# Optimization experiments

Hardware: AMD Instinct MI355X
Metric: run time of the kernel (lower is better)

Reference implementation:

```python
import jax, jax.numpy as jnp
import numpy as np

PAD = 0
C_CONST = 0.1712209


def setup_inputs() -> dict:
    key = jax.random.key(0)
    ks = jax.random.split(key, 6)
    tlen, bsz, slen, hsize, vocab = 64, 32, 64, 1024, 32000
    hidden = jax.random.normal(ks[0], (tlen, bsz, hsize), dtype=jnp.float32)
    context = jax.random.normal(ks[1], (slen, bsz, hsize), dtype=jnp.float32)
    src = jax.random.randint(ks[2], (bsz, slen), 0, vocab, dtype=jnp.int64)
    stdv = 1.0 / np.sqrt(hsize)
    W_gen = jax.random.uniform(ks[3], (vocab, hsize), dtype=jnp.float32, minval=-stdv, maxval=stdv)
    b_gen = jnp.zeros((vocab,), dtype=jnp.float32)
    # Xavier-like init for the copy gate
    w_copy = jax.random.normal(ks[4], (hsize,), dtype=jnp.float32) * np.sqrt(2.0 / (hsize + 1))
    b_copy = jnp.zeros((1,), dtype=jnp.float32)
    return {"hidden": hidden, "context": context, "src": src,
            "W_gen": W_gen, "b_gen": b_gen, "w_copy": w_copy, "b_copy": b_copy}


def reference(hidden, context, src, W_gen, b_gen, w_copy, b_copy):
    tlen, bsz, hsize = hidden.shape
    # p(z=1): probability of copying, [tlen, bsz, 1]
    copy_prob = jax.nn.sigmoid(jnp.einsum('tbh,h->tb', hidden, w_copy) + b_copy[0])[..., None]
    # generator distribution over tgt vocab
    logits = jnp.einsum('tbh,vh->tbv', hidden, W_gen) + b_gen
    prob = jax.nn.softmax(logits.astype(jnp.float32), axis=-1)
    p_g = prob * (1.0 - copy_prob)  # [tlen, bsz, vocab]
    # copy attention over source positions: bmm(query[b,t,h], keys[b,s,h]^T)
    attn_score = jnp.einsum('tbh,sbh->bts', hidden, context)  # [bsz, tlen, slen]
    src_mask = (src == PAD)[:, None, :]  # [bsz, 1, slen]
    attn_score = jnp.where(src_mask, -jnp.inf, attn_score.astype(jnp.float32))
    attns = jax.nn.softmax(attn_score, axis=-1)  # [bsz, tlen, slen]
    p_c = jnp.transpose(attns, (1, 0, 2)) * copy_prob  # [tlen, bsz, slen]
    # scatter_add copy probs into vocab distribution along dim 2
    slen = src.shape[1]
    idx_src = jnp.broadcast_to(src[None, :, :], (tlen, bsz, slen))
    t_idx = jnp.arange(tlen)[:, None, None]
    b_idx = jnp.arange(bsz)[None, :, None]
    p_g = p_g.at[t_idx, b_idx, idx_src].add(p_c)
    return jnp.log(p_g) + C_CONST
```

## Files before the change

### kernel.cpp

```cpp
#include <hip/hip_runtime.h>
#include <hip/hip_bf16.h>
#include <stdint.h>

#define TLEN 64
#define BSZ 32
#define SLEN 64
#define HS 1024
#define VOC 32000
#define NROW (TLEN*BSZ)
#define C_CONST_F 0.1712209f

#define BM 256
#define BN 256
#define BKT 32
#define NKT (HS/BKT)
#define SLOT_BYTES 32768
#define B_REGION 16384

typedef __attribute__((ext_vector_type(8))) short short8;
typedef __attribute__((ext_vector_type(4))) float f32x4;

static __device__ __forceinline__ ushort f2bf(float f) {
    uint32_t u = __builtin_bit_cast(uint32_t, f);
    uint32_t r = (u + 0x7fffu + ((u >> 16) & 1u)) >> 16;
    return (ushort)r;
}
static __device__ __forceinline__ float bf2f(ushort u) {
    uint32_t v = ((uint32_t)u) << 16;
    return __builtin_bit_cast(float, v);
}
static __device__ __forceinline__ void async16(const void* g, void* lds) {
    __builtin_amdgcn_global_load_lds(
        (const __attribute__((address_space(1))) void*)g,
        (__attribute__((address_space(3))) void*)lds, 16, 0, 0);
}
static __device__ __forceinline__ int swz12(int e) { return e ^ (((e >> 4) & 15) << 1); }

__global__ __launch_bounds__(256) void attn_kernel(const float* __restrict__ hidden,
                                                   const float* __restrict__ context,
                                                   const int* __restrict__ src,
                                                   const float* __restrict__ w_copy,
                                                   const float* __restrict__ b_copy,
                                                   float* __restrict__ cp,
                                                   float* __restrict__ p_c) {
    int row = blockIdx.x;
    int b = row & (BSZ - 1);
    int tid = threadIdx.x, wid = tid >> 6, lane = tid & 63;
    __shared__ float hrow[HS];
    __shared__ float sc[SLEN];
    __shared__ float wred[4];
    __shared__ float cp_s;
    float4 h4 = *(const float4*)(hidden + (size_t)row * HS + tid * 4);
    *(float4*)(hrow + tid * 4) = h4;
    float4 w4 = *(const float4*)(w_copy + tid * 4);
    float g = h4.x * w4.x + h4.y * w4.y + h4.z * w4.z + h4.w * w4.w;
    for (int m = 32; m >= 1; m >>= 1) g += __shfl_xor(g, m, 64);
    if (lane == 0) wred[wid] = g;
    __syncthreads();
    if (tid == 0) {
        float s = 1.f / (1.f + expf(-(wred[0] + wred[1] + wred[2] + wred[3] + b_copy[0])));
        cp_s = s;
        cp[row] = s;
    }
    for (int j = 0; j < 16; ++j) {
        int s = wid * 16 + j;
        const float* c = context + ((size_t)s * BSZ + b) * HS;
        float acc = 0.f;
        for (int i = 0; i < 4; ++i) {
            int off = (i * 64 + lane) * 4;
            float4 cv = *(const float4*)(c + off);
            float4 hv = *(const float4*)(hrow + off);
            acc += cv.x * hv.x + cv.y * hv.y + cv.z * hv.z + cv.w * hv.w;
        }
        for (int m = 32; m >= 1; m >>= 1) acc += __shfl_xor(acc, m, 64);
        if (lane == 0) sc[s] = acc;
    }
    __syncthreads();
    if (tid < SLEN) {
        float v = sc[tid];
        if (src[b * SLEN + tid] == 0) v = -INFINITY;
        float m = v;
        for (int k = 32; k >= 1; k >>= 1) m = fmaxf(m, __shfl_xor(m, k, 64));
        float e = expf(v - m);
        float ssum = e;
        for (int k = 32; k >= 1; k >>= 1) ssum += __shfl_xor(ssum, k, 64);
        p_c[row * SLEN + tid] = (e / ssum) * cp_s;
    }
}

__global__ __launch_bounds__(256) void cvt_kernel(const float* __restrict__ hidden,
                                                  const float* __restrict__ W_gen,
                                                  ushort* __restrict__ dst) {
    const int A4 = NROW * HS / 4;
    int i = blockIdx.x * 256 + threadIdx.x;
    float4 v = (i < A4) ? ((const float4*)hidden)[i] : ((const float4*)W_gen)[i - A4];
    ushort4 o;
    o.x = f2bf(v.x); o.y = f2bf(v.y); o.z = f2bf(v.z); o.w = f2bf(v.w);
    ((ushort4*)dst)[i] = o;
}

template <bool BF16L>
__global__ __launch_bounds__(512, 2) void gemm_kernel(const ushort* __restrict__ A,
                                                      const ushort* __restrict__ B,
                                                      const float* __restrict__ b_gen,
                                                      void* __restrict__ logits,
                                                      float* __restrict__ partials ) {
    __shared__ ushort sAB[4 * SLOT_BYTES / 2];

    int orig = blockIdx.x;
    int wg = (orig & 7) * 125 + (orig >> 3);
    int mIdx = wg & 7;
    int nIdx = wg >> 3;
    int m0 = mIdx * BM, n0 = nIdx * BN;
    int tid = threadIdx.x, wid = tid >> 6, lane = tid & 63;
    int wm = (wid >> 2) * 128, wn = (wid & 3) * 64;
    int lr = lane & 15, lg = lane >> 4;

    const ushort* gA[2]; const ushort* gB[2];
    uint32_t ldsOffA[2], ldsOffB[2];
    #pragma unroll
    for (int j = 0; j < 2; ++j) {
        int s = j * 512 + tid;
        int row = s >> 2;
        int kc = (s & 3) ^ ((row >> 1) & 3);
        gA[j] = A + (size_t)(m0 + row) * HS + kc * 8;
        gB[j] = B + (size_t)(n0 + row) * HS + kc * 8;
        ldsOffA[j] = (uint32_t)((j * 512 + wid * 64) * 16);
        ldsOffB[j] = (uint32_t)(B_REGION + (j * 512 + wid * 64) * 16);
    }

    uint32_t kcs   = (uint32_t)((lg ^ ((lr >> 1) & 3)) * 16);
    uint32_t offAb = (uint32_t)(wm + lr) * 64 + kcs;
    uint32_t offBb = B_REGION + (uint32_t)(wn + lr) * 64 + kcs;

    f32x4 acc[8][4];
    #pragma unroll
    for (int m = 0; m < 8; ++m)
        #pragma unroll
        for (int n = 0; n < 4; ++n) acc[m][n] = f32x4{0.f, 0.f, 0.f, 0.f};

#define STAGE(KT)                                                          \
    {                                                                      \
        char* sd = (char*)sAB + ((KT) & 3) * SLOT_BYTES;                   \
        int k0s = (KT) * BKT;                                              \
        _Pragma("unroll")                                                  \
        for (int j = 0; j < 2; ++j) {                                      \
            async16(gA[j] + k0s, sd + ldsOffA[j]);                         \
            async16(gB[j] + k0s, sd + ldsOffB[j]);                         \
        }                                                                  \
    }

#define PHASE_BODY(KT, DOSTAGE)                                                        \
    {                                                                                  \
        const char* sl = (const char*)sAB + ((KT) & 3) * SLOT_BYTES;                   \
        short8 af[8], bv[4];                                                           \
        _Pragma("unroll")                                                              \
        for (int mb = 0; mb < 8; ++mb)                                                 \
            af[mb] = *(const short8*)(sl + offAb + mb * 1024);                         \
        _Pragma("unroll")                                                              \
        for (int nb = 0; nb < 4; ++nb)                                                 \
            bv[nb] = *(const short8*)(sl + offBb + nb * 1024);                         \
        if (DOSTAGE) STAGE((KT) + 3);                                                  \
        _Pragma("unroll")                                                              \
        for (int mb = 0; mb < 8; ++mb)                                                 \
            _Pragma("unroll")                                                          \
            for (int nb = 0; nb < 4; ++nb)                                             \
                acc[mb][nb] = __builtin_amdgcn_mfma_f32_16x16x32_bf16(af[mb], bv[nb],  \
                                                                     acc[mb][nb], 0, 0, 0); \
    }

#define GATE8 asm volatile("s_waitcnt vmcnt(8)\n\ts_barrier" ::: "memory")

    STAGE(0); STAGE(1); STAGE(2);

    for (int kb = 0; kb < 7; ++kb) {
        int kt = kb * 4;
        GATE8; PHASE_BODY(kt + 0, true);
        GATE8; PHASE_BODY(kt + 1, true);
        GATE8; PHASE_BODY(kt + 2, true);
        GATE8; PHASE_BODY(kt + 3, true);
    }
    GATE8; PHASE_BODY(28, true);
    GATE8; PHASE_BODY(29, false);
    asm volatile("s_waitcnt vmcnt(4)\n\ts_barrier" ::: "memory");
    PHASE_BODY(30, false);
    asm volatile("s_waitcnt vmcnt(0)\n\ts_barrier" ::: "memory");
    PHASE_BODY(31, false);
#undef PHASE_BODY
#undef STAGE
#undef GATE8

    asm volatile("s_barrier" ::: "memory");

    float bg[4];
    #pragma unroll
    for (int nb = 0; nb < 4; ++nb) bg[nb] = b_gen[n0 + wn + nb * 16 + lr];
    int chunk = nIdx * 4 + (wid & 3);
    ushort* stile = sAB + wid * 8192;

    #pragma unroll
    for (int mb = 0; mb < 8; ++mb) {
        #pragma unroll
        for (int r = 0; r < 4; ++r) {
            int rl = mb * 16 + lg * 4 + r;
            int row = m0 + wm + rl;
            float v[4];
            float mx = -INFINITY;
            #pragma unroll
            for (int nb = 0; nb < 4; ++nb) {
                v[nb] = acc[mb][nb][r] + bg[nb];
                mx = fmaxf(mx, v[nb]);
            }
            if (BF16L) {
                #pragma unroll
                for (int nb = 0; nb < 4; ++nb) {
                    int cl = nb * 16 + lr;
                    int slot_w = (cl >> 3) ^ (rl & 7);
                    stile[rl * 64 + slot_w * 8 + (cl & 7)] = f2bf(v[nb]);
                }
            } else {
                float* outp = (float*)logits;
                #pragma unroll
                for (int nb = 0; nb < 4; ++nb)
                    outp[(size_t)row * VOC + n0 + wn + nb * 16 + lr] = v[nb];
            }
            for (int k = 8; k >= 1; k >>= 1) mx = fmaxf(mx, __shfl_xor(mx, k, 16));
            float se = 0.f;
            #pragma unroll
            for (int nb = 0; nb < 4; ++nb) se += __expf(v[nb] - mx);
            for (int k = 8; k >= 1; k >>= 1) se += __shfl_xor(se, k, 16);
            if (lr == 0) {
                float2 pv; pv.x = mx; pv.y = se;
                *(float2*)(partials + ((size_t)row * 500 + chunk) * 2) = pv;
            }
        }
    }
    if (BF16L) {
        ushort* Lbf = (ushort*)logits;
        #pragma unroll
        for (int rep = 0; rep < 16; ++rep) {
            int idx = rep * 64 + lane;
            int rl = idx >> 3, c8 = idx & 7;
            int slot_r = c8 ^ (rl & 7);
            short8 val = *(const short8*)(stile + rl * 64 + slot_r * 8);
            ushort* dst = Lbf + (size_t)(m0 + wm + rl) * VOC + n0 + wn + c8 * 8;
            *(short8*)dst = val;
        }
    }
}

__global__ __launch_bounds__(256) void reduce_kernel(const float* __restrict__ partials,
                                                     float* __restrict__ Ms,
                                                     float* __restrict__ Ss) {
    int wid = threadIdx.x >> 6, lane = threadIdx.x & 63;
    int row = blockIdx.x * 4 + wid;
    float m = -INFINITY, s = 0.f;
    for (int c = lane; c < 500; c += 64) {
        float2 p = *(const float2*)(partials + ((size_t)row * 500 + c) * 2);
        float nm = fmaxf(m, p.x);
        s = s * __expf(m - nm) + p.y * __expf(p.x - nm);
        m = nm;
    }
    for (int k = 32; k >= 1; k >>= 1) {
        float om = __shfl_xor(m, k, 64), os = __shfl_xor(s, k, 64);
        float nm = fmaxf(m, om);
        s = s * __expf(m - nm) + os * __expf(om - nm);
        m = nm;
    }
    if (lane == 0) { Ms[row] = m; Ss[row] = s; }
}

template <bool BF16L>
__global__ __launch_bounds__(256) void finalize_kernel(const int* __restrict__ src,
                                                       const float* __restrict__ p_c,
                                                       const float* __restrict__ cp,
                                                       const float* __restrict__ Ms,
                                                       const float* __restrict__ Ss,
                                                       const void* __restrict__ logits,
                                                       float* __restrict__ out) {
    int row = blockIdx.y;
    int c0 = blockIdx.x * 4096;
    int b = row & (BSZ - 1);
    __shared__ float addv[4096];
    int tid = threadIdx.x;
    for (int i = tid; i < 4096; i += 256) addv[i] = 0.f;
    __syncthreads();
    if (tid < SLEN) {
        int v = src[b * SLEN + tid];
        if (v >= c0 && v < c0 + 4096)
            atomicAdd(&addv[swz12(v - c0)], p_c[row * SLEN + tid]);
    }
    __syncthreads();
    int col = c0 + tid * 16;
    if (col >= VOC) return;
    float M = Ms[row];
    float g = (1.f - cp[row]) / Ss[row];
    float L[16];
    if (BF16L) {
        const ushort* lb = (const ushort*)logits + (size_t)row * VOC + col;
        short8 a = *(const short8*)lb;
        short8 c = *(const short8*)(lb + 8);
        for (int i = 0; i < 8; ++i) { L[i] = bf2f((ushort)a[i]); L[8 + i] = bf2f((ushort)c[i]); }
    } else {
        const float* lf = (const float*)logits + (size_t)row * VOC + col;
        for (int i = 0; i < 4; ++i) {
            float4 v = *(const float4*)(lf + i * 4);
            L[i * 4 + 0] = v.x; L[i * 4 + 1] = v.y; L[i * 4 + 2] = v.z; L[i * 4 + 3] = v.w;
        }
    }
    float res[16];
    for (int i = 0; i < 16; ++i) {
        float p = __expf(L[i] - M) * g + addv[swz12(tid * 16 + i)];
        res[i] = __logf(p) + C_CONST_F;
    }
    float* op = out + (size_t)row * VOC + col;
    for (int i = 0; i < 4; ++i) {
        float4 v;
        v.x = res[i * 4 + 0]; v.y = res[i * 4 + 1]; v.z = res[i * 4 + 2]; v.w = res[i * 4 + 3];
        *(float4*)(op + i * 4) = v;
    }
}

extern "C" void kernel_launch(void* const* d_in, const int* in_sizes, int n_in,
                              void* d_out, int out_size, void* d_ws, size_t ws_size,
                              hipStream_t stream) {
    const float* hidden  = (const float*)d_in[0];
    const float* context = (const float*)d_in[1];
    const int*   src     = (const int*)d_in[2];
    const float* W_gen   = (const float*)d_in[3];
    const float* b_gen   = (const float*)d_in[4];
    const float* w_copy  = (const float*)d_in[5];
    const float* b_copy  = (const float*)d_in[6];
    float* out = (float*)d_out;
    char* ws = (char*)d_ws;

    float*  cp       = (float*)(ws);
    float*  p_c      = (float*)(ws + 8192);
    float*  Ms       = (float*)(ws + 532480);
    float*  Ss       = (float*)(ws + 540672);
    float*  partials = (float*)(ws + 548864);
    ushort* Abf      = (ushort*)(ws + 8740864);
    ushort* Wbf      = (ushort*)(ws + 12935168);
    ushort* Lbf      = (ushort*)(ws + 78471168);
    const size_t NEED_BF16 = 209543168;
    (void)Wbf;

    attn_kernel<<<NROW, 256, 0, stream>>>(hidden, context, src, w_copy, b_copy, cp, p_c);
    cvt_kernel<<<(NROW * HS / 4 + VOC * HS / 4) / 256, 256, 0, stream>>>(hidden, W_gen, Abf);

    int ggrid = (NROW / BM) * (VOC / BN);
    dim3 fgrid(8, NROW);
    const ushort* Wb = (const ushort*)(ws + 12935168);
    if (ws_size >= NEED_BF16) {
        gemm_kernel<true><<<ggrid, 512, 0, stream>>>(Abf, Wb, b_gen, Lbf, partials);
        reduce_kernel<<<NROW / 4, 256, 0, stream>>>(partials, Ms, Ss);
        finalize_kernel<true><<<fgrid, 256, 0, stream>>>(src, p_c, cp, Ms, Ss, Lbf, out);
    } else {
        gemm_kernel<false><<<ggrid, 512, 0, stream>>>(Abf, Wb, b_gen, out, partials);
        reduce_kernel<<<NROW / 4, 256, 0, stream>>>(partials, Ms, Ss);
        finalize_kernel<false><<<fgrid, 256, 0, stream>>>(src, p_c, cp, Ms, Ss, out, out);
    }
}
```

Before: 334.6 us.

## Tile copy-attention on MFMA with split-bf16 and fold softmax reduce into finalize

The attention kernel now handles 16 target steps per block for one batch element. It stages hidden and context tiles through a triple-buffered LDS pipeline and computes the scores with bf16 MFMA using a hi/lo split, which keeps near-fp32 accuracy. This removes the old per-row reads of the whole context (64x1024 per row), at the cost of only 128 blocks. The separate reduce kernel is removed, and each finalize block now recombines the per-row max and sum partials itself, which drops one launch but repeats that small reduction 8 times per row.

```diff
diff --git a/kernel.cpp b/kernel.cpp
--- a/kernel.cpp
+++ b/kernel.cpp
@@ -43,48 +43,121 @@
                                                    const float* __restrict__ b_copy,
                                                    float* __restrict__ cp,
                                                    float* __restrict__ p_c) {
-    int row = blockIdx.x;
-    int b = row & (BSZ - 1);
+    int b  = blockIdx.x >> 2;
+    int tq = blockIdx.x & 3;
     int tid = threadIdx.x, wid = tid >> 6, lane = tid & 63;
-    __shared__ float hrow[HS];
-    __shared__ float sc[SLEN];
-    __shared__ float wred[4];
-    __shared__ float cp_s;
-    float4 h4 = *(const float4*)(hidden + (size_t)row * HS + tid * 4);
-    *(float4*)(hrow + tid * 4) = h4;
-    float4 w4 = *(const float4*)(w_copy + tid * 4);
-    float g = h4.x * w4.x + h4.y * w4.y + h4.z * w4.z + h4.w * w4.w;
-    for (int m = 32; m >= 1; m >>= 1) g += __shfl_xor(g, m, 64);
-    if (lane == 0) wred[wid] = g;
+    int lr = lane & 15, lg = lane >> 4;
+
+    __shared__ float hb[3][16][36];
+    __shared__ float cb[3][64][36];
+    __shared__ float wb[3][32];
+    __shared__ float sc[16][65];
+    __shared__ float gred[16];
+    __shared__ float cps[16];
+    __shared__ int   sbuf[SLEN];
+
+    if (tid < SLEN) sbuf[tid] = src[b * SLEN + tid];
+
+    const int cidx0 = tid * 2;
+    const int cs0 = cidx0 >> 3, ck0 = cidx0 & 7;
+    const int cs1 = (cidx0 + 1) >> 3, ck1 = (cidx0 + 1) & 7;
+    const float* cbase = context + (size_t)b * HS;
+    const float* hbase = hidden + ((size_t)(tq * 16) * 32 + b) * HS;
+
+    float4 rc0, rc1, rh, rw;
+#define ALOAD(I)                                                                   \
+    {                                                                              \
+        rc0 = *(const float4*)(cbase + (size_t)cs0 * 32 * HS + (I) * 32 + ck0 * 4);\
+        rc1 = *(const float4*)(cbase + (size_t)cs1 * 32 * HS + (I) * 32 + ck1 * 4);\
+        if (tid < 128) rh = *(const float4*)(hbase + (size_t)(tid >> 3) * 32 * HS + (I) * 32 + (tid & 7) * 4); \
+        if (tid < 8)  rw = *(const float4*)(w_copy + (I) * 32 + tid * 4);          \
+    }
+#define AWRITE(BUF)                                                                \
+    {                                                                              \
+        *(float4*)(&cb[BUF][cs0][ck0 * 4]) = rc0;                                  \
+        *(float4*)(&cb[BUF][cs1][ck1 * 4]) = rc1;                                  \
+        if (tid < 128) *(float4*)(&hb[BUF][tid >> 3][(tid & 7) * 4]) = rh;         \
+        if (tid < 8)  *(float4*)(&wb[BUF][tid * 4]) = rw;                          \
+    }
+
+    f32x4 acc = f32x4{0.f, 0.f, 0.f, 0.f};
+    float greg = 0.f;
+    int gt = lane >> 2, gk = lane & 3;
+
+    ALOAD(0); AWRITE(0);
+    ALOAD(1); AWRITE(1);
+    ALOAD(2);
     __syncthreads();
-    if (tid == 0) {
-        float s = 1.f / (1.f + expf(-(wred[0] + wred[1] + wred[2] + wred[3] + b_copy[0])));
-        cp_s = s;
-        cp[row] = s;
-    }
-    for (int j = 0; j < 16; ++j) {
-        int s = wid * 16 + j;
-        const float* c = context + ((size_t)s * BSZ + b) * HS;
-        float acc = 0.f;
+
+    for (int i = 0; i < 32; ++i) {
+        int buf = i % 3;
+        float4 a0 = *(const float4*)(&hb[buf][lr][lg * 8]);
+        float4 a1 = *(const float4*)(&hb[buf][lr][lg * 8 + 4]);
+        float4 b0 = *(const float4*)(&cb[buf][wid * 16 + lr][lg * 8]);
+        float4 b1 = *(const float4*)(&cb[buf][wid * 16 + lr][lg * 8 + 4]);
+        short8 ahi, alo, bhi, blo;
+        float af[8] = {a0.x, a0.y, a0.z, a0.w, a1.x, a1.y, a1.z, a1.w};
+        float bf[8] = {b0.x, b0.y, b0.z, b0.w, b1.x, b1.y, b1.z, b1.w};
+        #pragma unroll
+        for (int e = 0; e < 8; ++e) {
+            uint32_t ua = __builtin_bit_cast(uint32_t, af[e]);
+            ahi[e] = (short)(ua >> 16);
+            alo[e] = (short)f2bf(af[e] - __builtin_bit_cast(float, ua & 0xffff0000u));
+            uint32_t ub = __builtin_bit_cast(uint32_t, bf[e]);
+            bhi[e] = (short)(ub >> 16);
+            blo[e] = (short)f2bf(bf[e] - __builtin_bit_cast(float, ub & 0xffff0000u));
+        }
+        acc = __builtin_amdgcn_mfma_f32_16x16x32_bf16(ahi, bhi, acc, 0, 0, 0);
+        acc = __builtin_amdgcn_mfma_f32_16x16x32_bf16(ahi, blo, acc, 0, 0, 0);
+        acc = __builtin_amdgcn_mfma_f32_16x16x32_bf16(alo, bhi, acc, 0, 0, 0);
+        if (wid == 0) {
+            #pragma unroll
+            for (int e = 0; e < 8; ++e)
+                greg += hb[buf][gt][gk * 8 + e] * wb[buf][gk * 8 + e];
+        }
+        if (i + 2 < 32) {
+            AWRITE((i + 2) % 3);
+            if (i + 3 < 32) ALOAD(i + 3);
+        }
+        __syncthreads();
+    }
+#undef ALOAD
+#undef AWRITE
+
+    if (wid == 0) {
+        greg += __shfl_xor(greg, 1, 64);
+        greg += __shfl_xor(greg, 2, 64);
+        if (gk == 0) gred[gt] = greg;
+    }
+    #pragma unroll
+    for (int r = 0; r < 4; ++r)
+        sc[lg * 4 + r][wid * 16 + lr] = acc[r];
+    __syncthreads();
+    if (tid < 16) {
+        float s = 1.f / (1.f + expf(-(gred[tid] + b_copy[0])));
+        cps[tid] = s;
+        cp[(size_t)(tq * 16 + tid) * 32 + b] = s;
+    }
+    __syncthreads();
+    {
+        int t = tid >> 4, e = tid & 15;
+        float v[4];
+        float mx = -INFINITY;
+        #pragma unroll
         for (int i = 0; i < 4; ++i) {
-            int off = (i * 64 + lane) * 4;
-            float4 cv = *(const float4*)(c + off);
-            float4 hv = *(const float4*)(hrow + off);
-            acc += cv.x * hv.x + cv.y * hv.y + cv.z * hv.z + cv.w * hv.w;
-        }
-        for (int m = 32; m >= 1; m >>= 1) acc += __shfl_xor(acc, m, 64);
-        if (lane == 0) sc[s] = acc;
-    }
-    __syncthreads();
-    if (tid < SLEN) {
-        float v = sc[tid];
-        if (src[b * SLEN + tid] == 0) v = -INFINITY;
-        float m = v;
-        for (int k = 32; k >= 1; k >>= 1) m = fmaxf(m, __shfl_xor(m, k, 64));
-        float e = expf(v - m);
-        float ssum = e;
-        for (int k = 32; k >= 1; k >>= 1) ssum += __shfl_xor(ssum, k, 64);
-        p_c[row * SLEN + tid] = (e / ssum) * cp_s;
+            v[i] = sc[t][e * 4 + i];
+            if (sbuf[e * 4 + i] == 0) v[i] = -INFINITY;
+            mx = fmaxf(mx, v[i]);
+        }
+        for (int k = 8; k >= 1; k >>= 1) mx = fmaxf(mx, __shfl_xor(mx, k, 16));
+        float se = 0.f;
+        #pragma unroll
+        for (int i = 0; i < 4; ++i) { v[i] = __expf(v[i] - mx); se += v[i]; }
+        for (int k = 8; k >= 1; k >>= 1) se += __shfl_xor(se, k, 16);
+        float g = cps[t] / se;
+        int row = (tq * 16 + t) * 32 + b;
+        float4 o; o.x = v[0] * g; o.y = v[1] * g; o.z = v[2] * g; o.w = v[3] * g;
+        *(float4*)(p_c + (size_t)row * SLEN + e * 4) = o;
     }
 }
 
@@ -249,41 +322,36 @@
     }
 }
 
-__global__ __launch_bounds__(256) void reduce_kernel(const float* __restrict__ partials,
-                                                     float* __restrict__ Ms,
-                                                     float* __restrict__ Ss) {
-    int wid = threadIdx.x >> 6, lane = threadIdx.x & 63;
-    int row = blockIdx.x * 4 + wid;
-    float m = -INFINITY, s = 0.f;
-    for (int c = lane; c < 500; c += 64) {
-        float2 p = *(const float2*)(partials + ((size_t)row * 500 + c) * 2);
-        float nm = fmaxf(m, p.x);
-        s = s * __expf(m - nm) + p.y * __expf(p.x - nm);
-        m = nm;
-    }
-    for (int k = 32; k >= 1; k >>= 1) {
-        float om = __shfl_xor(m, k, 64), os = __shfl_xor(s, k, 64);
-        float nm = fmaxf(m, om);
-        s = s * __expf(m - nm) + os * __expf(om - nm);
-        m = nm;
-    }
-    if (lane == 0) { Ms[row] = m; Ss[row] = s; }
-}
-
 template <bool BF16L>
 __global__ __launch_bounds__(256) void finalize_kernel(const int* __restrict__ src,
                                                        const float* __restrict__ p_c,
                                                        const float* __restrict__ cp,
-                                                       const float* __restrict__ Ms,
-                                                       const float* __restrict__ Ss,
+                                                       const float* __restrict__ partials,
                                                        const void* __restrict__ logits,
                                                        float* __restrict__ out) {
     int row = blockIdx.y;
     int c0 = blockIdx.x * 4096;
     int b = row & (BSZ - 1);
     __shared__ float addv[4096];
+    __shared__ float MS[2];
     int tid = threadIdx.x;
     for (int i = tid; i < 4096; i += 256) addv[i] = 0.f;
+    if (tid < 64) {
+        float m = -INFINITY, s = 0.f;
+        for (int c = tid; c < 500; c += 64) {
+            float2 p = *(const float2*)(partials + ((size_t)row * 500 + c) * 2);
+            float nm = fmaxf(m, p.x);
+            s = s * __expf(m - nm) + p.y * __expf(p.x - nm);
+            m = nm;
+        }
+        for (int k = 32; k >= 1; k >>= 1) {
+            float om = __shfl_xor(m, k, 64), os = __shfl_xor(s, k, 64);
+            float nm = fmaxf(m, om);
+            s = s * __expf(m - nm) + os * __expf(om - nm);
+            m = nm;
+        }
+        if (tid == 0) { MS[0] = m; MS[1] = s; }
+    }
     __syncthreads();
     if (tid < SLEN) {
         int v = src[b * SLEN + tid];
@@ -293,8 +361,8 @@
     __syncthreads();
     int col = c0 + tid * 16;
     if (col >= VOC) return;
-    float M = Ms[row];
-    float g = (1.f - cp[row]) / Ss[row];
+    float M = MS[0];
+    float g = (1.f - cp[row]) / MS[1];
     float L[16];
     if (BF16L) {
         const ushort* lb = (const ushort*)logits + (size_t)row * VOC + col;
@@ -336,16 +404,12 @@
 
     float*  cp       = (float*)(ws);
     float*  p_c      = (float*)(ws + 8192);
-    float*  Ms       = (float*)(ws + 532480);
-    float*  Ss       = (float*)(ws + 540672);
     float*  partials = (float*)(ws + 548864);
     ushort* Abf      = (ushort*)(ws + 8740864);
-    ushort* Wbf      = (ushort*)(ws + 12935168);
+    const size_t NEED_BF16 = 209543168;
     ushort* Lbf      = (ushort*)(ws + 78471168);
-    const size_t NEED_BF16 = 209543168;
-    (void)Wbf;
-
-    attn_kernel<<<NROW, 256, 0, stream>>>(hidden, context, src, w_copy, b_copy, cp, p_c);
+
+    attn_kernel<<<BSZ * 4, 256, 0, stream>>>(hidden, context, src, w_copy, b_copy, cp, p_c);
     cvt_kernel<<<(NROW * HS / 4 + VOC * HS / 4) / 256, 256, 0, stream>>>(hidden, W_gen, Abf);
 
     int ggrid = (NROW / BM) * (VOC / BN);
@@ -353,11 +417,9 @@
     const ushort* Wb = (const ushort*)(ws + 12935168);
     if (ws_size >= NEED_BF16) {
         gemm_kernel<true><<<ggrid, 512, 0, stream>>>(Abf, Wb, b_gen, Lbf, partials);
-        reduce_kernel<<<NROW / 4, 256, 0, stream>>>(partials, Ms, Ss);
-        finalize_kernel<true><<<fgrid, 256, 0, stream>>>(src, p_c, cp, Ms, Ss, Lbf, out);
+        finalize_kernel<true><<<fgrid, 256, 0, stream>>>(src, p_c, cp, partials, Lbf, out);
     } else {
         gemm_kernel<false><<<ggrid, 512, 0, stream>>>(Abf, Wb, b_gen, out, partials);
-        reduce_kernel<<<NROW / 4, 256, 0, stream>>>(partials, Ms, Ss);
-        finalize_kernel<false><<<fgrid, 256, 0, stream>>>(src, p_c, cp, Ms, Ss, out, out);
-    }
-}
+        finalize_kernel<false><<<fgrid, 256, 0, stream>>>(src, p_c, cp, partials, out, out);
+    }
+}
```

Result: slower. 349.6 us (+4.5%).
